# Kernel tuning notes

Hardware: AMD Instinct MI355X
Metric: run time of the kernel (lower is better)

Reference implementation:

```python
import jax, jax.numpy as jnp
import numpy as np
from jax import lax

TAU = 1.0
GUMBEL_SCALE = 1e-4
SEARCH_SPACE = [1, 2, 4, 8, 16, 32, 64]


def synth_weight(weight, alphas_after):
    """Per-block circulant projection of weight for each block size, mixed by alphas.

    weight: [O, I, k, k]. For block size b: reshape to (q,b,p,b,k,k), rotate rows so
    each circulant diagonal aligns, mean over the block row axis, broadcast back with
    the reverse rotation, and accumulate alpha-weighted.
    """
    O, I, k, _ = weight.shape
    w = alphas_after[0] * weight  # block_size == 1 -> identity
    for idx, b in enumerate(SEARCH_SPACE[1:], start=1):
        q, p = O // b, I // b
        tmp = weight.reshape(q, b, p, b, k, k).transpose(0, 2, 1, 3, 4, 5)  # q,p,b,b,k,k
        ii = jnp.arange(b)[:, None]
        jj = jnp.arange(b)[None, :]
        rot = tmp[:, :, ii, (ii + jj) % b]          # q,p,b,b,k,k : rotate_mat gather
        cir = rot.mean(axis=2)                       # q,p,b,k,k   : circulant mean
        out = cir[:, :, (jj - ii) % b]               # q,p,b,b,k,k : rev_rotate_mat gather
        out = out.transpose(0, 2, 1, 3, 4, 5).reshape(O, I, k, k)
        w = w + alphas_after[idx] * out
    return w


def setup_inputs() -> dict:
    key = jax.random.key(0)
    k1, k2, k3 = jax.random.split(key, 3)
    B, C, H = 16, 256, 56
    O, I, K = 256, 256, 3
    x = jax.random.normal(k1, (B, C, H, H), dtype=jnp.float32)
    # kaiming-uniform-ish init: uniform in [-bound, bound], bound = sqrt(6/fan_in)
    fan_in = I * K * K
    bound = float(np.sqrt(6.0 / fan_in))
    weight = jax.random.uniform(k2, (O, I, K, K), dtype=jnp.float32, minval=-bound, maxval=bound)
    alphas = jnp.ones((len(SEARCH_SPACE),), dtype=jnp.float32)
    gumbels = jax.random.normal(k3, (len(SEARCH_SPACE),), dtype=jnp.float32)
    return {"x": x, "weight": weight, "alphas": alphas, "gumbels": gumbels}


def reference(x, weight, alphas, gumbels):
    # gumbel_softmax with tiny Gumbel(0, 1e-4) noise (noise passed in for determinism)
    alphas_after = jax.nn.softmax((alphas + GUMBEL_SCALE * gumbels) / TAU, axis=-1)
    w = synth_weight(weight, alphas_after)
    k = weight.shape[-1]
    pad = k // 2
    stride = 1
    out = lax.conv_general_dilated(
        x, w,
        window_strides=(stride, stride),
        padding=[(pad, pad), (pad, pad)],
        dimension_numbers=("NCHW", "OIHW", "NCHW"),
    )
    return out
```

## Files before the change

kernel.cpp:

```cpp
#include <hip/hip_runtime.h>
#include <hip/hip_bf16.h>

typedef __attribute__((ext_vector_type(8))) short bf16x8;
typedef __attribute__((ext_vector_type(4))) float f32x4;

#define WR_OFF   27557888

#define XBAND_SZ 24576
#define WBUF_OFF 49152
#define WBUF_SZ  16384

__global__ void wsynth_kernel(const float* __restrict__ W,
                              const float* __restrict__ alphas,
                              const float* __restrict__ gumbels,
                              __hip_bfloat16* __restrict__ Wr) {
    int tid = blockIdx.x * 256 + threadIdx.x;
    int o = tid >> 8, i = tid & 255;

    float a[7]; float mx = -1e30f;
    for (int j = 0; j < 7; ++j) { a[j] = alphas[j] + 1.0e-4f * gumbels[j]; mx = fmaxf(mx, a[j]); }
    float s = 0.f;
    for (int j = 0; j < 7; ++j) { a[j] = __expf(a[j] - mx); s += a[j]; }
    float invs = 1.0f / s;
    for (int j = 0; j < 7; ++j) a[j] *= invs;

    float acc[9];
    const float* w0 = W + ((size_t)(o * 256 + i)) * 9;
    for (int t = 0; t < 9; ++t) acc[t] = a[0] * w0[t];

    for (int idx = 1; idx < 7; ++idx) {
        int b = 1 << idx;
        int r = o & (b - 1), sc = i & (b - 1);
        int d = (sc - r) & (b - 1);
        int qb = o - r, pb = i - sc;
        float sum[9];
        for (int t = 0; t < 9; ++t) sum[t] = 0.f;
        for (int t = 0; t < b; ++t) {
            const float* wp = W + ((size_t)((qb + t) * 256 + pb + ((t + d) & (b - 1)))) * 9;
            #pragma unroll
            for (int tp = 0; tp < 9; ++tp) sum[tp] += wp[tp];
        }
        float sc2 = a[idx] / (float)b;
        for (int tp = 0; tp < 9; ++tp) acc[tp] += sc2 * sum[tp];
    }
    for (int tp = 0; tp < 9; ++tp)
        Wr[((size_t)(tp * 256 + o)) * 256 + i] = __float2bfloat16(acc[tp]);
}

__global__ void zero_border_kernel(__hip_bfloat16* __restrict__ Xp) {
    int t = blockIdx.x * 256 + threadIdx.x;
    int c = t & 255;
    int pp = t >> 8;
    int b = pp / 228;
    int p = pp - b * 228;
    int y, x;
    if (p < 58)       { y = 0;            x = p; }
    else if (p < 116) { y = 57;           x = p - 58; }
    else if (p < 172) { y = 1 + (p - 116); x = 0; }
    else              { y = 1 + (p - 172); x = 57; }
    Xp[((size_t)(b * 58 + y) * 58 + x) * 256 + c] = __float2bfloat16(0.f);
}

__global__ void pad_nhwc_kernel(const float* __restrict__ x,
                                __hip_bfloat16* __restrict__ Xp) {
    __shared__ float t[64][65];
    int p0 = blockIdx.x * 64;
    int c0 = blockIdx.y * 64;
    int b  = blockIdx.z;
    int lane = threadIdx.x & 63;
    int grp  = threadIdx.x >> 6;

    const float* src = x + ((size_t)(b * 256 + c0)) * 3136 + p0;
    #pragma unroll
    for (int it = 0; it < 16; ++it) {
        int c = it * 4 + grp;
        t[c][lane] = src[(size_t)c * 3136 + lane];
    }
    __syncthreads();
    #pragma unroll
    for (int it = 0; it < 16; ++it) {
        int pl = it * 4 + grp;
        int P = p0 + pl;
        int y = P / 56, xx = P - y * 56;
        Xp[(((size_t)(b * 58 + y + 1)) * 58 + (xx + 1)) * 256 + c0 + lane] =
            __float2bfloat16(t[lane][pl]);
    }
}

__device__ __forceinline__ void gload16(const __hip_bfloat16* g, char* l) {
    __builtin_amdgcn_global_load_lds(
        (const __attribute__((address_space(1))) void*)g,
        (__attribute__((address_space(3))) void*)l, 16, 0, 0);
}

template<int N> __device__ __forceinline__ void gate() {
    if constexpr (N == 0) asm volatile("s_waitcnt vmcnt(0)" ::: "memory");
    else if constexpr (N == 2) asm volatile("s_waitcnt vmcnt(2)" ::: "memory");
    else if constexpr (N == 4) asm volatile("s_waitcnt vmcnt(4)" ::: "memory");
    else if constexpr (N == 7) asm volatile("s_waitcnt vmcnt(7)" ::: "memory");
}

template<bool LAST>
__device__ __forceinline__ void chunk_body(
        char* smem, int cc,
        const int (&aOff)[4], const int (&bOff)[7],
        const __hip_bfloat16* wSrc0, const __hip_bfloat16* const (&xSrc)[3],
        int tid, f32x4 (&acc)[4][7])
{
    #pragma unroll
    for (int r = 0; r < 9; ++r) {
        const char* wb = smem + WBUF_OFF + ((cc + r) & 3) * WBUF_SZ;
        const char* xb = smem + (cc & 1) * XBAND_SZ;
        const int dy = r / 3 - 1, dx = r - (r / 3) * 3 - 1;
        const int timm = (dy * 64 + dx) * 16 + 1040;

        bf16x8 af[4], bf[4];
        #pragma unroll
        for (int nf = 0; nf < 4; ++nf) af[nf] = *(const bf16x8*)(wb + aOff[nf]);
        #pragma unroll
        for (int mf = 0; mf < 4; ++mf) bf[mf] = *(const bf16x8*)(xb + bOff[mf] + timm);

        if (!LAST || r < 6) {
            const int tap2 = (r + 3 < 9) ? r + 3 : r - 6;
            const int cc2  = (r + 3 < 9) ? cc : cc + 1;
            const __hip_bfloat16* s = wSrc0 + tap2 * 65536 + cc2 * 32;
            char* d = smem + WBUF_OFF + ((cc + r + 3) & 3) * WBUF_SZ + tid * 16;
            gload16(s, d);
            gload16(s + 16, d + 8192);
        }

        __builtin_amdgcn_s_barrier();
        asm volatile("s_waitcnt lgkmcnt(0)" ::: "memory");
        __builtin_amdgcn_s_setprio(1);
        #pragma unroll
        for (int nf = 0; nf < 4; ++nf)
            #pragma unroll
            for (int mf = 0; mf < 4; ++mf)
                acc[nf][mf] = __builtin_amdgcn_mfma_f32_16x16x32_bf16(
                    af[nf], bf[mf], acc[nf][mf], 0, 0, 0);
        __builtin_amdgcn_s_setprio(0);
        __builtin_amdgcn_s_barrier();

        bf16x8 bg[3];
        #pragma unroll
        for (int mf = 0; mf < 3; ++mf) bg[mf] = *(const bf16x8*)(xb + bOff[4 + mf] + timm);

        if (!LAST && r == 3) {
            char* d = smem + ((cc + 1) & 1) * XBAND_SZ + tid * 16;
            #pragma unroll
            for (int it = 0; it < 3; ++it)
                gload16(xSrc[it] + (cc + 1) * 32, d + it * 8192);
        }

        if constexpr (LAST) {
            if (r < 6) gate<4>();
            else if (r == 6) gate<2>();
            else if (r == 7) gate<0>();
        } else {
            if (r == 3 || r == 4 || r == 5) gate<7>();
            else gate<4>();
        }
        __builtin_amdgcn_s_barrier();
        asm volatile("s_waitcnt lgkmcnt(0)" ::: "memory");
        __builtin_amdgcn_s_setprio(1);
        #pragma unroll
        for (int nf = 0; nf < 4; ++nf)
            #pragma unroll
            for (int mf = 0; mf < 3; ++mf)
                acc[nf][4 + mf] = __builtin_amdgcn_mfma_f32_16x16x32_bf16(
                    af[nf], bg[mf], acc[nf][4 + mf], 0, 0, 0);
        __builtin_amdgcn_s_setprio(0);
        __builtin_amdgcn_s_barrier();
    }
}

__global__ __launch_bounds__(512, 2) void conv_kernel(
        const __hip_bfloat16* __restrict__ Xp,
        const __hip_bfloat16* __restrict__ Wr,
        float* __restrict__ out) {
    extern __shared__ char smem[];

    const int tid = threadIdx.x;
    const int w = tid >> 6, lane = tid & 63, l15 = lane & 15, q = lane >> 4;
    const int bid = blockIdx.x;
    const int bimg = bid / 14;
    const int y0 = (bid - bimg * 14) * 4;

    const int wn = (w & 3) << 6;
    const int wm = (w >> 2) * 112;

    const __hip_bfloat16* wSrc0 = Wr + (tid & 255) * 256 + (tid >> 8) * 8;

    const __hip_bfloat16* xSrc[3];
    #pragma unroll
    for (int it = 0; it < 3; ++it) {
        int chunk = tid + it * 512;
        int slot = chunk / 384;
        int rem  = chunk - slot * 384;
        int row = rem >> 6, xcol = rem & 63;
        xSrc[it] = Xp + (((size_t)(bimg * 58 + y0 + row)) * 58 + xcol) * 256 + slot * 8;
    }

    int aOff[4];
    #pragma unroll
    for (int nf = 0; nf < 4; ++nf) aOff[nf] = q * 4096 + (wn + nf * 16 + l15) * 16;
    int bOff[7];
    #pragma unroll
    for (int mf = 0; mf < 7; ++mf) {
        int p = wm + mf * 16 + l15;
        int y = p / 56, x = p - y * 56;
        bOff[mf] = q * 6144 + ((y + 1) * 64 + (x + 1)) * 16 - 1040;
    }

    f32x4 acc[4][7];
    #pragma unroll
    for (int a1 = 0; a1 < 4; ++a1)
        #pragma unroll
        for (int a2 = 0; a2 < 7; ++a2)
            acc[a1][a2] = (f32x4){0.f, 0.f, 0.f, 0.f};

    {
        char* d = smem + tid * 16;
        #pragma unroll
        for (int it = 0; it < 3; ++it) gload16(xSrc[it], d + it * 8192);
        #pragma unroll
        for (int t = 0; t < 3; ++t) {
            const __hip_bfloat16* s = wSrc0 + t * 65536;
            char* dw = smem + WBUF_OFF + t * WBUF_SZ + tid * 16;
            gload16(s, dw);
            gload16(s + 16, dw + 8192);
        }
    }
    gate<4>();
    __builtin_amdgcn_s_barrier();

    for (int cc = 0; cc < 7; ++cc)
        chunk_body<false>(smem, cc, aOff, bOff, wSrc0, xSrc, tid, acc);
    chunk_body<true>(smem, 7, aOff, bOff, wSrc0, xSrc, tid, acc);

    const int nb = wn + q * 4;
    const size_t obB = (size_t)bimg * 256 * 3136;
    #pragma unroll
    for (int mf = 0; mf < 7; ++mf) {
        int pm = y0 * 56 + wm + mf * 16 + l15;
        #pragma unroll
        for (int nf = 0; nf < 4; ++nf) {
            #pragma unroll
            for (int rr = 0; rr < 4; ++rr)
                out[obB + (size_t)(nb + nf * 16 + rr) * 3136 + pm] = acc[nf][mf][rr];
        }
    }
}

extern "C" void kernel_launch(void* const* d_in, const int* in_sizes, int n_in,
                              void* d_out, int out_size, void* d_ws, size_t ws_size,
                              hipStream_t stream) {
    const float* x       = (const float*)d_in[0];
    const float* weight  = (const float*)d_in[1];
    const float* alphas  = (const float*)d_in[2];
    const float* gumbels = (const float*)d_in[3];
    float* out = (float*)d_out;

    __hip_bfloat16* Xp = (__hip_bfloat16*)d_ws;
    __hip_bfloat16* Wr = (__hip_bfloat16*)((char*)d_ws + WR_OFF);

    hipFuncSetAttribute(reinterpret_cast<const void*>(conv_kernel),
                        hipFuncAttributeMaxDynamicSharedMemorySize, 114688);

    hipLaunchKernelGGL(zero_border_kernel, dim3(3648),      dim3(256), 0, stream, Xp);
    hipLaunchKernelGGL(wsynth_kernel,      dim3(256),       dim3(256), 0, stream,
                       weight, alphas, gumbels, Wr);
    hipLaunchKernelGGL(pad_nhwc_kernel,    dim3(49, 4, 16), dim3(256), 0, stream, x, Xp);
    hipLaunchKernelGGL(conv_kernel,        dim3(224),       dim3(512), 114688, stream,
                       Xp, Wr, out);
}
```

Before: 110.7 us.

## Fuse fp32-to-bf16 padding into conv kernel and stream weights directly from global

Drops the separate zero-border and NHWC pad/convert kernels. The conv kernel now reads fp32 NCHW input directly, zero-pads out-of-bounds pixels in registers, converts to bf16 and writes the band to LDS with a register-staged double buffer. Weight fragments are loaded straight from global/L2 into registers with one-tap-ahead prefetch instead of going through LDS, which cuts LDS to 48KB and removes most barriers. The trade-off is uncoalesced strided fp32 gathers across channels and exposed global latency on the weight loads.

```diff
diff --git a/kernel.cpp b/kernel.cpp
--- a/kernel.cpp
+++ b/kernel.cpp
@@ -4,11 +4,7 @@
 typedef __attribute__((ext_vector_type(8))) short bf16x8;
 typedef __attribute__((ext_vector_type(4))) float f32x4;
 
-#define WR_OFF   27557888
-
-#define XBAND_SZ 24576
-#define WBUF_OFF 49152
-#define WBUF_SZ  16384
+#define BAND 24576
 
 __global__ void wsynth_kernel(const float* __restrict__ W,
                               const float* __restrict__ alphas,
@@ -47,138 +43,113 @@
         Wr[((size_t)(tp * 256 + o)) * 256 + i] = __float2bfloat16(acc[tp]);
 }
 
-__global__ void zero_border_kernel(__hip_bfloat16* __restrict__ Xp) {
-    int t = blockIdx.x * 256 + threadIdx.x;
-    int c = t & 255;
-    int pp = t >> 8;
-    int b = pp / 228;
-    int p = pp - b * 228;
-    int y, x;
-    if (p < 58)       { y = 0;            x = p; }
-    else if (p < 116) { y = 57;           x = p - 58; }
-    else if (p < 172) { y = 1 + (p - 116); x = 0; }
-    else              { y = 1 + (p - 172); x = 57; }
-    Xp[((size_t)(b * 58 + y) * 58 + x) * 256 + c] = __float2bfloat16(0.f);
-}
-
-__global__ void pad_nhwc_kernel(const float* __restrict__ x,
-                                __hip_bfloat16* __restrict__ Xp) {
-    __shared__ float t[64][65];
-    int p0 = blockIdx.x * 64;
-    int c0 = blockIdx.y * 64;
-    int b  = blockIdx.z;
-    int lane = threadIdx.x & 63;
-    int grp  = threadIdx.x >> 6;
-
-    const float* src = x + ((size_t)(b * 256 + c0)) * 3136 + p0;
-    #pragma unroll
-    for (int it = 0; it < 16; ++it) {
-        int c = it * 4 + grp;
-        t[c][lane] = src[(size_t)c * 3136 + lane];
-    }
-    __syncthreads();
-    #pragma unroll
-    for (int it = 0; it < 16; ++it) {
-        int pl = it * 4 + grp;
-        int P = p0 + pl;
-        int y = P / 56, xx = P - y * 56;
-        Xp[(((size_t)(b * 58 + y + 1)) * 58 + (xx + 1)) * 256 + c0 + lane] =
-            __float2bfloat16(t[lane][pl]);
-    }
-}
-
-__device__ __forceinline__ void gload16(const __hip_bfloat16* g, char* l) {
-    __builtin_amdgcn_global_load_lds(
-        (const __attribute__((address_space(1))) void*)g,
-        (__attribute__((address_space(3))) void*)l, 16, 0, 0);
-}
-
-template<int N> __device__ __forceinline__ void gate() {
-    if constexpr (N == 0) asm volatile("s_waitcnt vmcnt(0)" ::: "memory");
-    else if constexpr (N == 2) asm volatile("s_waitcnt vmcnt(2)" ::: "memory");
-    else if constexpr (N == 4) asm volatile("s_waitcnt vmcnt(4)" ::: "memory");
-    else if constexpr (N == 7) asm volatile("s_waitcnt vmcnt(7)" ::: "memory");
+union BFPack { short s[8]; bf16x8 v; };
+
+__device__ __forceinline__ bf16x8 pack8(const float* f) {
+    BFPack p;
+    #pragma unroll
+    for (int j = 0; j < 8; ++j) {
+        __hip_bfloat16 h = __float2bfloat16(f[j]);
+        p.s[j] = *reinterpret_cast<short*>(&h);
+    }
+    return p.v;
+}
+
+__device__ __forceinline__ void stage_load(const float* __restrict__ xb, int ch0, int y0,
+                                           int g, int px, bf16x8 (&sv)[3]) {
+    #pragma unroll
+    for (int rr = 0; rr < 3; ++rr) {
+        int pxt = px + rr * 128;
+        int row = y0 - 1 + (pxt >> 6);
+        int col = (pxt & 63) - 1;
+        bool ok = ((unsigned)row < 56u) && ((unsigned)col < 56u);
+        int rowc = row < 0 ? 0 : (row > 55 ? 55 : row);
+        int colc = col < 0 ? 0 : (col > 55 ? 55 : col);
+        const float* p = xb + (size_t)(ch0 + g * 8) * 3136 + rowc * 56 + colc;
+        float tmp[8];
+        #pragma unroll
+        for (int j = 0; j < 8; ++j) {
+            float v = p[(size_t)j * 3136];
+            tmp[j] = ok ? v : 0.f;
+        }
+        sv[rr] = pack8(tmp);
+    }
+}
+
+__device__ __forceinline__ void stage_write(char* dst, int g, int px, const bf16x8 (&sv)[3]) {
+    #pragma unroll
+    for (int rr = 0; rr < 3; ++rr)
+        *reinterpret_cast<bf16x8*>(dst + g * 6144 + (px + rr * 128) * 16) = sv[rr];
 }
 
 template<bool LAST>
-__device__ __forceinline__ void chunk_body(
-        char* smem, int cc,
-        const int (&aOff)[4], const int (&bOff)[7],
-        const __hip_bfloat16* wSrc0, const __hip_bfloat16* const (&xSrc)[3],
-        int tid, f32x4 (&acc)[4][7])
+__device__ __forceinline__ void chunk_pair(
+    int cp, char* smem, const float* __restrict__ xb,
+    const __hip_bfloat16* const (&aPtr)[4],
+    const int (&bOff)[7], int y0, int g, int px,
+    bf16x8 (&afr)[2][4], bf16x8 (&bfA)[2][4],
+    f32x4 (&acc)[4][7])
 {
-    #pragma unroll
-    for (int r = 0; r < 9; ++r) {
-        const char* wb = smem + WBUF_OFF + ((cc + r) & 3) * WBUF_SZ;
-        const char* xb = smem + (cc & 1) * XBAND_SZ;
-        const int dy = r / 3 - 1, dx = r - (r / 3) * 3 - 1;
-        const int timm = (dy * 64 + dx) * 16 + 1040;
-
-        bf16x8 af[4], bf[4];
-        #pragma unroll
-        for (int nf = 0; nf < 4; ++nf) af[nf] = *(const bf16x8*)(wb + aOff[nf]);
-        #pragma unroll
-        for (int mf = 0; mf < 4; ++mf) bf[mf] = *(const bf16x8*)(xb + bOff[mf] + timm);
-
-        if (!LAST || r < 6) {
-            const int tap2 = (r + 3 < 9) ? r + 3 : r - 6;
-            const int cc2  = (r + 3 < 9) ? cc : cc + 1;
-            const __hip_bfloat16* s = wSrc0 + tap2 * 65536 + cc2 * 32;
-            char* d = smem + WBUF_OFF + ((cc + r + 3) & 3) * WBUF_SZ + tid * 16;
-            gload16(s, d);
-            gload16(s + 16, d + 8192);
-        }
-
-        __builtin_amdgcn_s_barrier();
-        asm volatile("s_waitcnt lgkmcnt(0)" ::: "memory");
-        __builtin_amdgcn_s_setprio(1);
-        #pragma unroll
-        for (int nf = 0; nf < 4; ++nf)
-            #pragma unroll
-            for (int mf = 0; mf < 4; ++mf)
-                acc[nf][mf] = __builtin_amdgcn_mfma_f32_16x16x32_bf16(
-                    af[nf], bf[mf], acc[nf][mf], 0, 0, 0);
-        __builtin_amdgcn_s_setprio(0);
-        __builtin_amdgcn_s_barrier();
-
-        bf16x8 bg[3];
-        #pragma unroll
-        for (int mf = 0; mf < 3; ++mf) bg[mf] = *(const bf16x8*)(xb + bOff[4 + mf] + timm);
-
-        if (!LAST && r == 3) {
-            char* d = smem + ((cc + 1) & 1) * XBAND_SZ + tid * 16;
-            #pragma unroll
-            for (int it = 0; it < 3; ++it)
-                gload16(xSrc[it] + (cc + 1) * 32, d + it * 8192);
-        }
-
-        if constexpr (LAST) {
-            if (r < 6) gate<4>();
-            else if (r == 6) gate<2>();
-            else if (r == 7) gate<0>();
-        } else {
-            if (r == 3 || r == 4 || r == 5) gate<7>();
-            else gate<4>();
-        }
-        __builtin_amdgcn_s_barrier();
-        asm volatile("s_waitcnt lgkmcnt(0)" ::: "memory");
-        __builtin_amdgcn_s_setprio(1);
-        #pragma unroll
-        for (int nf = 0; nf < 4; ++nf)
+    const int cp64 = cp * 64;
+    #pragma unroll
+    for (int u = 0; u < 2; ++u) {
+        bf16x8 sv[3];
+        #pragma unroll
+        for (int r = 0; r < 9; ++r) {
+            const int cur = (u + r) & 1, nxt = cur ^ 1;
+            const int dy = r / 3 - 1, dx = r % 3 - 1;
+            const int timm = (dy * 64 + dx) * 16;
+            const char* bandCur = smem + u * BAND;
+
+            if (!(LAST && u == 1 && r == 8)) {
+                const int tapn = (r == 8) ? 0 : r + 1;
+                const int eoff = tapn * 65536 + (u + (r == 8 ? 1 : 0)) * 32;
+                #pragma unroll
+                for (int nf = 0; nf < 4; ++nf)
+                    afr[nxt][nf] = *(const bf16x8*)(aPtr[nf] + cp64 + eoff);
+                const int dyn = tapn / 3 - 1, dxn = tapn % 3 - 1;
+                const int timn = (dyn * 64 + dxn) * 16;
+                const char* bandN = smem + ((r == 8) ? (u ^ 1) : u) * BAND;
+                #pragma unroll
+                for (int mf = 0; mf < 4; ++mf)
+                    bfA[nxt][mf] = *(const bf16x8*)(bandN + bOff[mf] + timn);
+            }
+            bf16x8 bfB[3];
             #pragma unroll
             for (int mf = 0; mf < 3; ++mf)
-                acc[nf][4 + mf] = __builtin_amdgcn_mfma_f32_16x16x32_bf16(
-                    af[nf], bg[mf], acc[nf][4 + mf], 0, 0, 0);
-        __builtin_amdgcn_s_setprio(0);
-        __builtin_amdgcn_s_barrier();
+                bfB[mf] = *(const bf16x8*)(bandCur + bOff[4 + mf] + timm);
+
+            if (r == 0 && !(LAST && u == 1))
+                stage_load(xb, (2 * cp + u + 1) * 32, y0, g, px, sv);
+
+            __builtin_amdgcn_s_setprio(1);
+            #pragma unroll
+            for (int nf = 0; nf < 4; ++nf)
+                #pragma unroll
+                for (int mf = 0; mf < 4; ++mf)
+                    acc[nf][mf] = __builtin_amdgcn_mfma_f32_16x16x32_bf16(
+                        afr[cur][nf], bfA[cur][mf], acc[nf][mf], 0, 0, 0);
+            #pragma unroll
+            for (int nf = 0; nf < 4; ++nf)
+                #pragma unroll
+                for (int mf = 0; mf < 3; ++mf)
+                    acc[nf][4 + mf] = __builtin_amdgcn_mfma_f32_16x16x32_bf16(
+                        afr[cur][nf], bfB[mf], acc[nf][4 + mf], 0, 0, 0);
+            __builtin_amdgcn_s_setprio(0);
+
+            if (r == 6 && !(LAST && u == 1))
+                stage_write(smem + (u ^ 1) * BAND, g, px, sv);
+            if (r == 7 && !(LAST && u == 1))
+                __syncthreads();
+        }
     }
 }
 
 __global__ __launch_bounds__(512, 2) void conv_kernel(
-        const __hip_bfloat16* __restrict__ Xp,
+        const float* __restrict__ x,
         const __hip_bfloat16* __restrict__ Wr,
         float* __restrict__ out) {
-    extern __shared__ char smem[];
+    __shared__ char smem[2 * BAND];
 
     const int tid = threadIdx.x;
     const int w = tid >> 6, lane = tid & 63, l15 = lane & 15, q = lane >> 4;
@@ -188,28 +159,21 @@
 
     const int wn = (w & 3) << 6;
     const int wm = (w >> 2) * 112;
-
-    const __hip_bfloat16* wSrc0 = Wr + (tid & 255) * 256 + (tid >> 8) * 8;
-
-    const __hip_bfloat16* xSrc[3];
-    #pragma unroll
-    for (int it = 0; it < 3; ++it) {
-        int chunk = tid + it * 512;
-        int slot = chunk / 384;
-        int rem  = chunk - slot * 384;
-        int row = rem >> 6, xcol = rem & 63;
-        xSrc[it] = Xp + (((size_t)(bimg * 58 + y0 + row)) * 58 + xcol) * 256 + slot * 8;
-    }
-
-    int aOff[4];
-    #pragma unroll
-    for (int nf = 0; nf < 4; ++nf) aOff[nf] = q * 4096 + (wn + nf * 16 + l15) * 16;
+    const int g = tid >> 7, px = tid & 127;
+
+    const float* xb = x + (size_t)bimg * 256 * 3136;
+
+    const __hip_bfloat16* aPtr[4];
+    #pragma unroll
+    for (int nf = 0; nf < 4; ++nf)
+        aPtr[nf] = Wr + (wn + nf * 16 + l15) * 256 + q * 8;
+
     int bOff[7];
     #pragma unroll
     for (int mf = 0; mf < 7; ++mf) {
         int p = wm + mf * 16 + l15;
-        int y = p / 56, x = p - y * 56;
-        bOff[mf] = q * 6144 + ((y + 1) * 64 + (x + 1)) * 16 - 1040;
+        int y = p / 56, xx = p - y * 56;
+        bOff[mf] = q * 6144 + ((y + 1) * 64 + (xx + 1)) * 16;
     }
 
     f32x4 acc[4][7];
@@ -219,24 +183,25 @@
         for (int a2 = 0; a2 < 7; ++a2)
             acc[a1][a2] = (f32x4){0.f, 0.f, 0.f, 0.f};
 
+    bf16x8 afr[2][4], bfA[2][4];
+
     {
-        char* d = smem + tid * 16;
-        #pragma unroll
-        for (int it = 0; it < 3; ++it) gload16(xSrc[it], d + it * 8192);
-        #pragma unroll
-        for (int t = 0; t < 3; ++t) {
-            const __hip_bfloat16* s = wSrc0 + t * 65536;
-            char* dw = smem + WBUF_OFF + t * WBUF_SZ + tid * 16;
-            gload16(s, dw);
-            gload16(s + 16, dw + 8192);
-        }
-    }
-    gate<4>();
-    __builtin_amdgcn_s_barrier();
-
-    for (int cc = 0; cc < 7; ++cc)
-        chunk_body<false>(smem, cc, aOff, bOff, wSrc0, xSrc, tid, acc);
-    chunk_body<true>(smem, 7, aOff, bOff, wSrc0, xSrc, tid, acc);
+        bf16x8 sv[3];
+        stage_load(xb, 0, y0, g, px, sv);
+        stage_write(smem, g, px, sv);
+    }
+    __syncthreads();
+    {
+        const int timm = (-64 - 1) * 16;
+        #pragma unroll
+        for (int nf = 0; nf < 4; ++nf) afr[0][nf] = *(const bf16x8*)(aPtr[nf]);
+        #pragma unroll
+        for (int mf = 0; mf < 4; ++mf) bfA[0][mf] = *(const bf16x8*)(smem + bOff[mf] + timm);
+    }
+
+    for (int cp = 0; cp < 3; ++cp)
+        chunk_pair<false>(cp, smem, xb, aPtr, bOff, y0, g, px, afr, bfA, acc);
+    chunk_pair<true>(3, smem, xb, aPtr, bOff, y0, g, px, afr, bfA, acc);
 
     const int nb = wn + q * 4;
     const size_t obB = (size_t)bimg * 256 * 3136;
@@ -261,16 +226,10 @@
     const float* gumbels = (const float*)d_in[3];
     float* out = (float*)d_out;
 
-    __hip_bfloat16* Xp = (__hip_bfloat16*)d_ws;
-    __hip_bfloat16* Wr = (__hip_bfloat16*)((char*)d_ws + WR_OFF);
-
-    hipFuncSetAttribute(reinterpret_cast<const void*>(conv_kernel),
-                        hipFuncAttributeMaxDynamicSharedMemorySize, 114688);
-
-    hipLaunchKernelGGL(zero_border_kernel, dim3(3648),      dim3(256), 0, stream, Xp);
-    hipLaunchKernelGGL(wsynth_kernel,      dim3(256),       dim3(256), 0, stream,
+    __hip_bfloat16* Wr = (__hip_bfloat16*)d_ws;
+
+    hipLaunchKernelGGL(wsynth_kernel, dim3(256), dim3(256), 0, stream,
                        weight, alphas, gumbels, Wr);
-    hipLaunchKernelGGL(pad_nhwc_kernel,    dim3(49, 4, 16), dim3(256), 0, stream, x, Xp);
-    hipLaunchKernelGGL(conv_kernel,        dim3(224),       dim3(512), 114688, stream,
-                       Xp, Wr, out);
-}
+    hipLaunchKernelGGL(conv_kernel,   dim3(224), dim3(512), 0, stream,
+                       x, Wr, out);
+}
```

After: 147.0 us (median of 2 runs). +32.8%, slower.

## Precompute circulant diagonal sums and collapse conv MFMA phases per tap

Applied to the files above, without the earlier changes.

Adds a diagsum kernel that computes each circulant diagonal sum once per block level into workspace (aliased over the padded-input buffer, which is written later). The weight synthesis then reads one precomputed sum per level instead of re-summing up to 64 weight rows per output element, removing heavily redundant global reads. The conv inner loop is restructured to issue all 7 B-fragment loads and all 28 MFMAs per tap in one phase, dropping the split two-phase scheme and most of the barriers and explicit lgkmcnt waits. This raises register pressure and relies on the existing vmcnt gates and a single barrier per tap for correctness.

```diff
diff --git a/kernel.cpp b/kernel.cpp
--- a/kernel.cpp
+++ b/kernel.cpp
@@ -6,13 +6,41 @@
 
 #define WR_OFF   27557888
 
-#define XBAND_SZ 24576
+#define BAND     24576
 #define WBUF_OFF 49152
 #define WBUF_SZ  16384
+
+__global__ void diagsum_kernel(const float* __restrict__ W, float* __restrict__ S) {
+    int t = blockIdx.x * 256 + threadIdx.x;
+    int idx, n, lvlOff;
+    if (t < 32768)      { idx = 1; n = t;          lvlOff = 0; }
+    else if (t < 49152) { idx = 2; n = t - 32768;  lvlOff = 294912; }
+    else if (t < 57344) { idx = 3; n = t - 49152;  lvlOff = 442368; }
+    else if (t < 61440) { idx = 4; n = t - 57344;  lvlOff = 516096; }
+    else if (t < 63488) { idx = 5; n = t - 61440;  lvlOff = 552960; }
+    else                { idx = 6; n = t - 63488;  lvlOff = 571392; }
+    int b = 1 << idx;
+    int d = n & (b - 1);
+    int qp = n >> idx;
+    int p = qp & ((256 >> idx) - 1);
+    int q = qp >> (8 - idx);
+    float s[9];
+    #pragma unroll
+    for (int tp = 0; tp < 9; ++tp) s[tp] = 0.f;
+    for (int tt = 0; tt < b; ++tt) {
+        const float* wp = W + ((size_t)((q * b + tt) * 256 + p * b + ((tt + d) & (b - 1)))) * 9;
+        #pragma unroll
+        for (int tp = 0; tp < 9; ++tp) s[tp] += wp[tp];
+    }
+    float* o = S + (size_t)lvlOff + (size_t)n * 9;
+    #pragma unroll
+    for (int tp = 0; tp < 9; ++tp) o[tp] = s[tp];
+}
 
 __global__ void wsynth_kernel(const float* __restrict__ W,
                               const float* __restrict__ alphas,
                               const float* __restrict__ gumbels,
+                              const float* __restrict__ S,
                               __hip_bfloat16* __restrict__ Wr) {
     int tid = blockIdx.x * 256 + threadIdx.x;
     int o = tid >> 8, i = tid & 255;
@@ -26,23 +54,22 @@
 
     float acc[9];
     const float* w0 = W + ((size_t)(o * 256 + i)) * 9;
+    #pragma unroll
     for (int t = 0; t < 9; ++t) acc[t] = a[0] * w0[t];
 
+    const int lvlOff[7] = {0, 0, 294912, 442368, 516096, 552960, 571392};
+    int dif = i - o;
+    #pragma unroll
     for (int idx = 1; idx < 7; ++idx) {
         int b = 1 << idx;
-        int r = o & (b - 1), sc = i & (b - 1);
-        int d = (sc - r) & (b - 1);
-        int qb = o - r, pb = i - sc;
-        float sum[9];
-        for (int t = 0; t < 9; ++t) sum[t] = 0.f;
-        for (int t = 0; t < b; ++t) {
-            const float* wp = W + ((size_t)((qb + t) * 256 + pb + ((t + d) & (b - 1)))) * 9;
-            #pragma unroll
-            for (int tp = 0; tp < 9; ++tp) sum[tp] += wp[tp];
-        }
-        float sc2 = a[idx] / (float)b;
-        for (int tp = 0; tp < 9; ++tp) acc[tp] += sc2 * sum[tp];
-    }
+        int q = o >> idx, p = i >> idx, d = dif & (b - 1);
+        int n = ((q * (256 >> idx) + p) << idx) + d;
+        const float* sp = S + lvlOff[idx] + (size_t)n * 9;
+        float sc = a[idx] / (float)b;
+        #pragma unroll
+        for (int tp = 0; tp < 9; ++tp) acc[tp] += sc * sp[tp];
+    }
+    #pragma unroll
     for (int tp = 0; tp < 9; ++tp)
         Wr[((size_t)(tp * 256 + o)) * 256 + i] = __float2bfloat16(acc[tp]);
 }
@@ -94,7 +121,7 @@
 }
 
 template<int N> __device__ __forceinline__ void gate() {
-    if constexpr (N == 0) asm volatile("s_waitcnt vmcnt(0)" ::: "memory");
+    if constexpr (N == 0)      asm volatile("s_waitcnt vmcnt(0)" ::: "memory");
     else if constexpr (N == 2) asm volatile("s_waitcnt vmcnt(2)" ::: "memory");
     else if constexpr (N == 4) asm volatile("s_waitcnt vmcnt(4)" ::: "memory");
     else if constexpr (N == 7) asm volatile("s_waitcnt vmcnt(7)" ::: "memory");
@@ -102,75 +129,53 @@
 
 template<bool LAST>
 __device__ __forceinline__ void chunk_body(
-        char* smem, int cc,
-        const int (&aOff)[4], const int (&bOff)[7],
-        const __hip_bfloat16* wSrc0, const __hip_bfloat16* const (&xSrc)[3],
-        int tid, f32x4 (&acc)[4][7])
+    int cc, char* smem,
+    const int (&aOff)[4], const int (&bOff)[7],
+    const __hip_bfloat16* wSrc0, const __hip_bfloat16* const (&xSrc)[3],
+    int tid, f32x4 (&acc)[4][7])
 {
+    const char* xb = smem + (cc & 1) * BAND;
     #pragma unroll
     for (int r = 0; r < 9; ++r) {
-        const char* wb = smem + WBUF_OFF + ((cc + r) & 3) * WBUF_SZ;
-        const char* xb = smem + (cc & 1) * XBAND_SZ;
-        const int dy = r / 3 - 1, dx = r - (r / 3) * 3 - 1;
-        const int timm = (dy * 64 + dx) * 16 + 1040;
-
-        bf16x8 af[4], bf[4];
-        #pragma unroll
-        for (int nf = 0; nf < 4; ++nf) af[nf] = *(const bf16x8*)(wb + aOff[nf]);
-        #pragma unroll
-        for (int mf = 0; mf < 4; ++mf) bf[mf] = *(const bf16x8*)(xb + bOff[mf] + timm);
-
-        if (!LAST || r < 6) {
-            const int tap2 = (r + 3 < 9) ? r + 3 : r - 6;
-            const int cc2  = (r + 3 < 9) ? cc : cc + 1;
+        if (!LAST || r <= 5) {
+            const int tap2 = (r < 6) ? r + 3 : r - 6;
+            const int cc2  = (r < 6) ? cc : cc + 1;
             const __hip_bfloat16* s = wSrc0 + tap2 * 65536 + cc2 * 32;
             char* d = smem + WBUF_OFF + ((cc + r + 3) & 3) * WBUF_SZ + tid * 16;
             gload16(s, d);
             gload16(s + 16, d + 8192);
         }
-
-        __builtin_amdgcn_s_barrier();
-        asm volatile("s_waitcnt lgkmcnt(0)" ::: "memory");
-        __builtin_amdgcn_s_setprio(1);
-        #pragma unroll
-        for (int nf = 0; nf < 4; ++nf)
-            #pragma unroll
-            for (int mf = 0; mf < 4; ++mf)
-                acc[nf][mf] = __builtin_amdgcn_mfma_f32_16x16x32_bf16(
-                    af[nf], bf[mf], acc[nf][mf], 0, 0, 0);
-        __builtin_amdgcn_s_setprio(0);
-        __builtin_amdgcn_s_barrier();
-
-        bf16x8 bg[3];
-        #pragma unroll
-        for (int mf = 0; mf < 3; ++mf) bg[mf] = *(const bf16x8*)(xb + bOff[4 + mf] + timm);
-
         if (!LAST && r == 3) {
-            char* d = smem + ((cc + 1) & 1) * XBAND_SZ + tid * 16;
+            char* d = smem + ((cc + 1) & 1) * BAND + tid * 16;
             #pragma unroll
             for (int it = 0; it < 3; ++it)
                 gload16(xSrc[it] + (cc + 1) * 32, d + it * 8192);
         }
-
+        const char* wb = smem + WBUF_OFF + ((cc + r) & 3) * WBUF_SZ;
+        const int dy = r / 3 - 1, dx = r % 3 - 1;
+        const int timm = (dy * 64 + dx) * 16;
+        bf16x8 af[4], bfv[7];
+        #pragma unroll
+        for (int nf = 0; nf < 4; ++nf) af[nf] = *(const bf16x8*)(wb + aOff[nf]);
+        #pragma unroll
+        for (int mf = 0; mf < 7; ++mf) bfv[mf] = *(const bf16x8*)(xb + bOff[mf] + timm);
+        __builtin_amdgcn_s_setprio(1);
+        #pragma unroll
+        for (int nf = 0; nf < 4; ++nf)
+            #pragma unroll
+            for (int mf = 0; mf < 7; ++mf)
+                acc[nf][mf] = __builtin_amdgcn_mfma_f32_16x16x32_bf16(
+                    af[nf], bfv[mf], acc[nf][mf], 0, 0, 0);
+        __builtin_amdgcn_s_setprio(0);
         if constexpr (LAST) {
-            if (r < 6) gate<4>();
+            if (r <= 5)      gate<4>();
             else if (r == 6) gate<2>();
             else if (r == 7) gate<0>();
         } else {
             if (r == 3 || r == 4 || r == 5) gate<7>();
-            else gate<4>();
-        }
-        __builtin_amdgcn_s_barrier();
-        asm volatile("s_waitcnt lgkmcnt(0)" ::: "memory");
-        __builtin_amdgcn_s_setprio(1);
-        #pragma unroll
-        for (int nf = 0; nf < 4; ++nf)
-            #pragma unroll
-            for (int mf = 0; mf < 3; ++mf)
-                acc[nf][4 + mf] = __builtin_amdgcn_mfma_f32_16x16x32_bf16(
-                    af[nf], bg[mf], acc[nf][4 + mf], 0, 0, 0);
-        __builtin_amdgcn_s_setprio(0);
-        __builtin_amdgcn_s_barrier();
+            else                            gate<4>();
+        }
+        if (!(LAST && r == 8)) __builtin_amdgcn_s_barrier();
     }
 }
 
@@ -208,8 +213,8 @@
     #pragma unroll
     for (int mf = 0; mf < 7; ++mf) {
         int p = wm + mf * 16 + l15;
-        int y = p / 56, x = p - y * 56;
-        bOff[mf] = q * 6144 + ((y + 1) * 64 + (x + 1)) * 16 - 1040;
+        int y = p / 56, xx = p - y * 56;
+        bOff[mf] = q * 6144 + ((y + 1) * 64 + (xx + 1)) * 16;
     }
 
     f32x4 acc[4][7];
@@ -235,8 +240,8 @@
     __builtin_amdgcn_s_barrier();
 
     for (int cc = 0; cc < 7; ++cc)
-        chunk_body<false>(smem, cc, aOff, bOff, wSrc0, xSrc, tid, acc);
-    chunk_body<true>(smem, 7, aOff, bOff, wSrc0, xSrc, tid, acc);
+        chunk_body<false>(cc, smem, aOff, bOff, wSrc0, xSrc, tid, acc);
+    chunk_body<true>(7, smem, aOff, bOff, wSrc0, xSrc, tid, acc);
 
     const int nb = wn + q * 4;
     const size_t obB = (size_t)bimg * 256 * 3136;
@@ -262,14 +267,17 @@
     float* out = (float*)d_out;
 
     __hip_bfloat16* Xp = (__hip_bfloat16*)d_ws;
+    float*          S  = (float*)d_ws;
     __hip_bfloat16* Wr = (__hip_bfloat16*)((char*)d_ws + WR_OFF);
 
     hipFuncSetAttribute(reinterpret_cast<const void*>(conv_kernel),
                         hipFuncAttributeMaxDynamicSharedMemorySize, 114688);
 
+    hipLaunchKernelGGL(diagsum_kernel,     dim3(252),       dim3(256), 0, stream,
+                       weight, S);
+    hipLaunchKernelGGL(wsynth_kernel,      dim3(256),       dim3(256), 0, stream,
+                       weight, alphas, gumbels, S, Wr);
     hipLaunchKernelGGL(zero_border_kernel, dim3(3648),      dim3(256), 0, stream, Xp);
-    hipLaunchKernelGGL(wsynth_kernel,      dim3(256),       dim3(256), 0, stream,
-                       weight, alphas, gumbels, Wr);
     hipLaunchKernelGGL(pad_nhwc_kernel,    dim3(49, 4, 16), dim3(256), 0, stream, x, Xp);
     hipLaunchKernelGGL(conv_kernel,        dim3(224),       dim3(512), 114688, stream,
                        Xp, Wr, out);
```

Result: no change. 111.0 us (+0.3%).
